# Kernel tuning notes

Hardware: AMD Instinct MI355X
Metric: run time of the kernel (lower is better)

Reference implementation:

```python
import jax, jax.numpy as jnp
import numpy as np

B, N, OUT = 32, 2048, 100

def setup_inputs() -> dict:
    key = jax.random.key(0)
    k1, k2 = jax.random.split(key)
    query = jax.random.normal(k1, (B, N), dtype=jnp.float32) * 10.0
    # Dense(100, use_bias=False) kernel, glorot-ish scale
    W = jax.random.normal(k2, (N, OUT), dtype=jnp.float32) * (1.0 / np.sqrt(N))
    return {"query": query, "W": W}

def reference(query, W):
    # Faithful translation of the TF graph:
    # cast -> expand_dims(1)/(2) -> broadcast add -> cast -> reduce_sum(axis=1)
    c = query.astype(jnp.int32)                      # [B, N]
    g = c[:, None, :] + c[:, :, None]                # [B, N, N], g[b,i,j] = c[b,j] + c[b,i]
    f = g.astype(jnp.float32)
    f_reduced = jnp.sum(f, axis=1)                   # [B, N] == N*c[b,j] + sum_i c[b,i]
    diff = query - f_reduced
    rem = diff * diff                                # squared diff
    return rem @ W                                   # [B, 100]
```

## Files before the change

kernel.cpp:

```cpp
#include <hip/hip_runtime.h>

#define BATCH  32
#define NDIM   2048
#define NOUT   100
#define SPLIT  8
#define SLICE  (NDIM / SPLIT)
#define BLOCK  256

__global__ __launch_bounds__(BLOCK)
void fused_model_kernel(const float* __restrict__ q,
                        const float* __restrict__ W,
                        float* __restrict__ out)
{
    const int s = blockIdx.x;
    const int b = blockIdx.y;
    const int t = threadIdx.x;

    __shared__ float rem_lds[SLICE];
    __shared__ int   red[BLOCK];
    __shared__ float half_partial[128];

    const float* qrow = q + b * NDIM;

    int   csum  = 0;
    float q_mine = 0.f;
    int   c_mine = 0;
    #pragma unroll
    for (int k = 0; k < SPLIT; ++k) {
        float v = qrow[k * SLICE + t];
        int   c = (int)v;
        csum += c;
        if (k == s) { q_mine = v; c_mine = c; }
    }
    red[t] = csum;
    __syncthreads();
    #pragma unroll
    for (int w = BLOCK / 2; w > 0; w >>= 1) {
        if (t < w) red[t] += red[t + w];
        __syncthreads();
    }
    const int S = red[0];

    {
        float d = q_mine - (float)(NDIM * c_mine + S);
        rem_lds[t] = d * d;
    }
    __syncthreads();

    const int o = t & 127;
    const int h = t >> 7;
    float acc = 0.f;
    if (o < NOUT) {
        const int jbeg = h * (SLICE / 2);
        const float* Wbase = W + (size_t)(s * SLICE) * NOUT + o;
        #pragma unroll 4
        for (int j = 0; j < SLICE / 2; ++j) {
            acc += rem_lds[jbeg + j] * Wbase[(size_t)(jbeg + j) * NOUT];
        }
    }
    if (h == 1 && o < NOUT) half_partial[o] = acc;
    __syncthreads();
    if (h == 0 && o < NOUT) {
        acc += half_partial[o];
        atomicAdd(&out[b * NOUT + o], acc);
    }
}

extern "C" void kernel_launch(void* const* d_in, const int* in_sizes, int n_in,
                              void* d_out, int out_size, void* d_ws, size_t ws_size,
                              hipStream_t stream) {
    const float* q = (const float*)d_in[0];
    const float* W = (const float*)d_in[1];
    float* out = (float*)d_out;

    hipMemsetAsync(out, 0, (size_t)out_size * sizeof(float), stream);

    dim3 grid(SPLIT, BATCH);
    fused_model_kernel<<<grid, BLOCK, 0, stream>>>(q, W, out);
}
```

Baseline: 65.66 us.

## Double split count and replace LDS tree reduction with wave shuffles

The N dimension is now split across 16 blocks per batch row instead of 8, doubling the grid to 512 blocks so more CUs share the W streaming. The row-sum reduction moves from an 8-step LDS tree with a barrier per step to wave-level shuffle-xor plus a tiny cross-wave sum, cutting synchronisation. The matvec inner loop unroll goes from 4 to 8. In exchange, each block still reads the whole query row for the sum, so redundant reads double, and twice as many atomics hit the output.

```diff
diff --git a/kernel.cpp b/kernel.cpp
--- a/kernel.cpp
+++ b/kernel.cpp
@@ -3,7 +3,7 @@
 #define BATCH  32
 #define NDIM   2048
 #define NOUT   100
-#define SPLIT  8
+#define SPLIT  16
 #define SLICE  (NDIM / SPLIT)
 #define BLOCK  256
 
@@ -17,32 +17,35 @@
     const int t = threadIdx.x;
 
     __shared__ float rem_lds[SLICE];
-    __shared__ int   red[BLOCK];
+    __shared__ int   wave_sum[BLOCK / 64];
     __shared__ float half_partial[128];
+    __shared__ int   S_lds;
 
     const float* qrow = q + b * NDIM;
 
-    int   csum  = 0;
-    float q_mine = 0.f;
-    int   c_mine = 0;
+    int csum = 0;
     #pragma unroll
-    for (int k = 0; k < SPLIT; ++k) {
-        float v = qrow[k * SLICE + t];
+    for (int k = 0; k < NDIM / BLOCK; ++k)
+        csum += (int)qrow[k * BLOCK + t];
+
+    #pragma unroll
+    for (int m = 32; m > 0; m >>= 1)
+        csum += __shfl_xor(csum, m, 64);
+    if ((t & 63) == 0) wave_sum[t >> 6] = csum;
+    __syncthreads();
+    if (t == 0) {
+        int ssum = 0;
+        #pragma unroll
+        for (int w = 0; w < BLOCK / 64; ++w) ssum += wave_sum[w];
+        S_lds = ssum;
+    }
+    __syncthreads();
+    const int S = S_lds;
+
+    if (t < SLICE) {
+        float v = qrow[s * SLICE + t];
         int   c = (int)v;
-        csum += c;
-        if (k == s) { q_mine = v; c_mine = c; }
-    }
-    red[t] = csum;
-    __syncthreads();
-    #pragma unroll
-    for (int w = BLOCK / 2; w > 0; w >>= 1) {
-        if (t < w) red[t] += red[t + w];
-        __syncthreads();
-    }
-    const int S = red[0];
-
-    {
-        float d = q_mine - (float)(NDIM * c_mine + S);
+        float d = v - (float)(NDIM * c + S);
         rem_lds[t] = d * d;
     }
     __syncthreads();
@@ -52,10 +55,10 @@
     float acc = 0.f;
     if (o < NOUT) {
         const int jbeg = h * (SLICE / 2);
-        const float* Wbase = W + (size_t)(s * SLICE) * NOUT + o;
-        #pragma unroll 4
+        const float* Wbase = W + (size_t)(s * SLICE + jbeg) * NOUT + o;
+        #pragma unroll 8
         for (int j = 0; j < SLICE / 2; ++j) {
-            acc += rem_lds[jbeg + j] * Wbase[(size_t)(jbeg + j) * NOUT];
+            acc += rem_lds[jbeg + j] * Wbase[(size_t)j * NOUT];
         }
     }
     if (h == 1 && o < NOUT) half_partial[o] = acc;
```

New measurement: 60.03 us. 8.6% less time.
